# Kernel tuning notes

Hardware: AMD Instinct MI355X
Metric: run time of the kernel (lower is better)

## Reference

```python
import jax, jax.numpy as jnp
import numpy as np

# geomloss SamplesLoss(loss='sinkhorn', p=2, blur=0.05, scaling=0.8) constants
P = 2
BLUR = 0.05
SCALING = 0.8
# inputs are L2-normalized, so the point-cloud diameter is bounded by 2
DIAMETER = 2.0


def _eps_list():
    # geomloss epsilon_schedule: anneal eps from diameter**p down to blur**p
    e = [DIAMETER ** P]
    e += [float(np.exp(v)) for v in np.arange(P * np.log(DIAMETER), P * np.log(BLUR), P * np.log(SCALING))]
    e += [BLUR ** P]
    return e


def _cost(a, b):
    # geomloss p=2 cost: 0.5 * squared Euclidean distance, shape [N, M]
    sq = jnp.sum(a * a, -1)[:, None] + jnp.sum(b * b, -1)[None, :] - 2.0 * (a @ b.T)
    return 0.5 * jnp.maximum(sq, 0.0)


def _softmin(eps, C, h):
    # h = log-weights + potential/eps over the reduced axis; returns [N]
    return -eps * jax.nn.logsumexp(h[None, :] - C / eps, axis=1)


def _sinkhorn_divergence(x, y):
    # Debiased Sinkhorn divergence with epsilon-scaling (geomloss sinkhorn_tensorized)
    sg = jax.lax.stop_gradient
    N, M = x.shape[0], y.shape[0]
    a_log = jnp.full((N,), -np.log(N), x.dtype)  # uniform weights 1/N (log)
    b_log = jnp.full((M,), -np.log(M), y.dtype)

    C_xy = _cost(x, y)
    C_yx = C_xy.T
    C_xx = _cost(x, x)
    C_yy = _cost(y, y)
    # Sinkhorn loop runs without gradient (envelope theorem), like torch no_grad
    D_xy, D_yx, D_xx, D_yy = sg(C_xy), sg(C_yx), sg(C_xx), sg(C_yy)

    eps_list = _eps_list()
    eps = eps_list[0]
    g_ab = _softmin(eps, D_yx, a_log)   # potential on y for OT(a, b)
    f_ba = _softmin(eps, D_xy, b_log)   # potential on x for OT(a, b)
    f_aa = _softmin(eps, D_xx, a_log)   # debiasing potential OT(a, a)
    g_bb = _softmin(eps, D_yy, b_log)   # debiasing potential OT(b, b)

    for eps in eps_list:
        ft_ba = _softmin(eps, D_xy, b_log + g_ab / eps)
        gt_ab = _softmin(eps, D_yx, a_log + f_ba / eps)
        ft_aa = _softmin(eps, D_xx, a_log + f_aa / eps)
        gt_bb = _softmin(eps, D_yy, b_log + g_bb / eps)
        f_ba = 0.5 * (f_ba + ft_ba)
        g_ab = 0.5 * (g_ab + gt_ab)
        f_aa = 0.5 * (f_aa + ft_aa)
        g_bb = 0.5 * (g_bb + gt_bb)

    # final extrapolation with gradients enabled, dual potentials detached
    eps = eps_list[-1]
    f_ba, g_ab = (
        _softmin(eps, C_xy, sg(b_log + g_ab / eps)),
        _softmin(eps, C_yx, sg(a_log + f_ba / eps)),
    )
    f_aa = _softmin(eps, C_xx, sg(a_log + f_aa / eps))
    g_bb = _softmin(eps, C_yy, sg(b_log + g_bb / eps))

    # S_eps(a,b) = <a, f_ba - f_aa> + <b, g_ab - g_bb>, uniform weights
    return jnp.mean(f_ba - f_aa) + jnp.mean(g_ab - g_bb)


def setup_inputs() -> dict:
    key = jax.random.key(0)
    kx, ky = jax.random.split(key)
    x = jax.random.normal(kx, (4096, 64), jnp.float32)
    y = jax.random.normal(ky, (4096, 64), jnp.float32)
    return {"x": x, "y": y}


def reference(x, y):
    x = x / jnp.linalg.norm(x, axis=1, keepdims=True)
    y = y / jnp.linalg.norm(y, axis=1, keepdims=True)
    return _sinkhorn_divergence(x, y)
```

## Files before the change

kernel.cpp:

```cpp
#include <hip/hip_runtime.h>
#include <math.h>

#define NPTS 4096
#define DIM 64
#define NM ((size_t)NPTS * (size_t)NPTS)
#define LOGW (-8.317766166719343f)
#define NEGINF (-__builtin_inff())

typedef __bf16 bf16x8 __attribute__((ext_vector_type(8)));
typedef float f32x4 __attribute__((ext_vector_type(4)));
typedef _Float16 half8 __attribute__((ext_vector_type(8)));

static __device__ __forceinline__ f32x4 mfma16(bf16x8 a, bf16x8 b, f32x4 c) {
  return __builtin_amdgcn_mfma_f32_16x16x32_bf16(a, b, c, 0, 0, 0);
}

__global__ __launch_bounds__(256) void norm_split_kernel(
    const float* __restrict__ x, const float* __restrict__ y,
    __bf16* __restrict__ xh, __bf16* __restrict__ xl,
    __bf16* __restrict__ yh, __bf16* __restrict__ yl) {
  int row  = blockIdx.x * 4 + (threadIdx.x >> 6);
  int lane = threadIdx.x & 63;
  const float* src; __bf16 *dh, *dl;
  if (row < NPTS) {
    src = x + (size_t)row * DIM; dh = xh + (size_t)row * DIM; dl = xl + (size_t)row * DIM;
  } else {
    int r = row - NPTS;
    src = y + (size_t)r * DIM; dh = yh + (size_t)r * DIM; dl = yl + (size_t)r * DIM;
  }
  float v = src[lane];
  float s = v * v;
  #pragma unroll
  for (int o = 32; o; o >>= 1) s += __shfl_xor(s, o, 64);
  v *= 1.0f / sqrtf(s);
  __bf16 h = (__bf16)v;
  __bf16 l = (__bf16)(v - (float)h);
  dh[lane] = h;
  dl[lane] = l;
}

__global__ __launch_bounds__(256) void cost_mfma_kernel(
    const __bf16* __restrict__ xh, const __bf16* __restrict__ xl,
    const __bf16* __restrict__ yh, const __bf16* __restrict__ yl,
    _Float16* __restrict__ Cw) {
  int mat = blockIdx.z;
  const __bf16 *Ah, *Al, *Bh, *Bl;
  if (mat == 0)      { Ah = xh; Al = xl; Bh = yh; Bl = yl; }
  else if (mat == 1) { Ah = yh; Al = yl; Bh = xh; Bl = xl; }
  else if (mat == 2) { Ah = xh; Al = xl; Bh = xh; Bl = xl; }
  else               { Ah = yh; Al = yl; Bh = yh; Bl = yl; }
  _Float16* Cout = Cw + (size_t)mat * NM;

  int i0 = blockIdx.y * 64, j0 = blockIdx.x * 64;
  int wave = threadIdx.x >> 6, L = threadIdx.x & 63;
  int mrow = L & 15, quad = L >> 4;

  size_t abase = (size_t)(i0 + wave * 16 + mrow) * DIM + quad * 8;
  bf16x8 ah0 = *(const bf16x8*)(Ah + abase);
  bf16x8 ah1 = *(const bf16x8*)(Ah + abase + 32);
  bf16x8 al0 = *(const bf16x8*)(Al + abase);
  bf16x8 al1 = *(const bf16x8*)(Al + abase + 32);

  #pragma unroll
  for (int ct = 0; ct < 4; ++ct) {
    size_t bbase = (size_t)(j0 + ct * 16 + mrow) * DIM + quad * 8;
    bf16x8 bh0 = *(const bf16x8*)(Bh + bbase);
    bf16x8 bh1 = *(const bf16x8*)(Bh + bbase + 32);
    bf16x8 bl0 = *(const bf16x8*)(Bl + bbase);
    bf16x8 bl1 = *(const bf16x8*)(Bl + bbase + 32);
    f32x4 acc = {0.0f, 0.0f, 0.0f, 0.0f};
    acc = mfma16(ah0, bh0, acc);
    acc = mfma16(ah1, bh1, acc);
    acc = mfma16(al0, bh0, acc);
    acc = mfma16(al1, bh1, acc);
    acc = mfma16(ah0, bl0, acc);
    acc = mfma16(ah1, bl1, acc);
    int gj = j0 + ct * 16 + mrow;
    #pragma unroll
    for (int q = 0; q < 4; ++q) {
      int gi = i0 + wave * 16 + quad * 4 + q;
      Cout[(size_t)gi * NPTS + gj] = (_Float16)fmaxf(1.0f - acc[q], 0.0f);
    }
  }
}

__global__ __launch_bounds__(256) void pass_kernel(
    const _Float16* __restrict__ Cw,
    const float* __restrict__ potOld, float* __restrict__ potNew,
    float inv_eps, float eps, int use_pot, int avg) {
  int blk  = blockIdx.x;
  int mat  = blk >> 10;
  int row  = (blk & 1023) * 4 + (threadIdx.x >> 6);
  int lane = threadIdx.x & 63;
  const _Float16* Crow = Cw + (size_t)mat * NM + (size_t)row * NPTS;
  int ridx = (mat == 0) ? 1 : ((mat == 1) ? 0 : mat);
  const float* pot = potOld + (size_t)ridx * NPTS;

  float m0 = NEGINF, s0 = 0.0f, m1 = NEGINF, s1 = 0.0f;
  #pragma unroll 2
  for (int t = 0; t < 8; ++t) {
    int j = lane * 8 + t * 512;
    half8 c8 = *(const half8*)(Crow + j);
    float h[8];
    if (use_pot) {
      float4 pa = *(const float4*)(pot + j);
      float4 pb = *(const float4*)(pot + j + 4);
      h[0] = fmaf(pa.x, inv_eps, LOGW); h[1] = fmaf(pa.y, inv_eps, LOGW);
      h[2] = fmaf(pa.z, inv_eps, LOGW); h[3] = fmaf(pa.w, inv_eps, LOGW);
      h[4] = fmaf(pb.x, inv_eps, LOGW); h[5] = fmaf(pb.y, inv_eps, LOGW);
      h[6] = fmaf(pb.z, inv_eps, LOGW); h[7] = fmaf(pb.w, inv_eps, LOGW);
    } else {
      #pragma unroll
      for (int e = 0; e < 8; ++e) h[e] = LOGW;
    }
    #pragma unroll
    for (int e = 0; e < 8; e += 2) {
      float tv = fmaf((float)c8[e], -inv_eps, h[e]);
      float mn = fmaxf(m0, tv);
      s0 = s0 * __expf(m0 - mn) + __expf(tv - mn);
      m0 = mn;
      float tv1 = fmaf((float)c8[e + 1], -inv_eps, h[e + 1]);
      float mn1 = fmaxf(m1, tv1);
      s1 = s1 * __expf(m1 - mn1) + __expf(tv1 - mn1);
      m1 = mn1;
    }
  }
  {
    float mn = fmaxf(m0, m1);
    s0 = s0 * __expf(m0 - mn) + s1 * __expf(m1 - mn);
    m0 = mn;
  }
  #pragma unroll
  for (int o = 1; o < 64; o <<= 1) {
    float m2 = __shfl_xor(m0, o, 64);
    float s2 = __shfl_xor(s0, o, 64);
    float mn = fmaxf(m0, m2);
    s0 = s0 * __expf(m0 - mn) + s2 * __expf(m2 - mn);
    m0 = mn;
  }
  if (lane == 0) {
    float ft = -eps * (m0 + __logf(s0));
    float v = avg ? 0.5f * (potOld[(size_t)mat * NPTS + row] + ft) : ft;
    potNew[(size_t)mat * NPTS + row] = v;
  }
}

__global__ __launch_bounds__(256) void final_kernel(
    const float* __restrict__ pot, float* __restrict__ out) {
  __shared__ float red[256];
  float s = 0.0f;
  for (int j = threadIdx.x; j < NPTS; j += 256)
    s += (pot[j] - pot[2 * NPTS + j]) + (pot[NPTS + j] - pot[3 * NPTS + j]);
  red[threadIdx.x] = s;
  __syncthreads();
  #pragma unroll
  for (int o = 128; o; o >>= 1) {
    if (threadIdx.x < o) red[threadIdx.x] += red[threadIdx.x + o];
    __syncthreads();
  }
  if (threadIdx.x == 0) out[0] = red[0] / (float)NPTS;
}

extern "C" void kernel_launch(void* const* d_in, const int* in_sizes, int n_in,
                              void* d_out, int out_size, void* d_ws, size_t ws_size,
                              hipStream_t stream) {
  const float* x = (const float*)d_in[0];
  const float* y = (const float*)d_in[1];
  char* ws = (char*)d_ws;

  _Float16* Cw = (_Float16*)ws;
  __bf16* xh = (__bf16*)(ws + 4 * NM * sizeof(_Float16));
  __bf16* xl = xh + (size_t)NPTS * DIM;
  __bf16* yh = xl + (size_t)NPTS * DIM;
  __bf16* yl = yh + (size_t)NPTS * DIM;
  float* potA = (float*)(yl + (size_t)NPTS * DIM);
  float* potB = potA + 4 * (size_t)NPTS;
  size_t needed = (size_t)((char*)(potB + 4 * (size_t)NPTS) - ws);
  if (ws_size < needed) return;

  norm_split_kernel<<<2048, 256, 0, stream>>>(x, y, xh, xl, yh, yl);
  cost_mfma_kernel<<<dim3(64, 64, 4), 256, 0, stream>>>(xh, xl, yh, yl, Cw);

  double lst[32];
  int c = 0;
  lst[c++] = 4.0;
  double start = 2.0 * log(2.0), stop = 2.0 * log(0.05), step = 2.0 * log(0.8);
  for (int k = 0;; ++k) {
    double v = start + (double)k * step;
    if (v <= stop) break;
    lst[c++] = exp(v);
  }
  lst[c++] = 0.05 * 0.05;

  for (int p = 0; p < c + 2; ++p) {
    double e = (p == 0) ? lst[0] : ((p <= c) ? lst[p - 1] : lst[c - 1]);
    float eps = (float)e;
    float inv_eps = 1.0f / eps;
    int use_pot = (p > 0) ? 1 : 0;
    int avg = (p >= 1 && p <= c) ? 1 : 0;
    const float* po = (p & 1) ? potB : potA;
    float* pn       = (p & 1) ? potA : potB;
    pass_kernel<<<4096, 256, 0, stream>>>(Cw, po, pn, inv_eps, eps, use_pot, avg);
  }
  final_kernel<<<1, 256, 0, stream>>>(potB, (float*)d_out);
}
```

Measured before the change: 819.3 us.

## Fuse cost-matrix computation into each Sinkhorn pass, dropping stored cost matrices

Removes the precomputed fp16 cost matrices and recomputes the split-bf16 MFMA dot products inside each softmin pass, feeding an online logsumexp with a lazy max-rescale threshold. Each block handles 64 rows with the A fragments held in registers, streams B rows with one-step prefetch, and merges results across waves through LDS. This trades roughly 128 MB of HBM traffic per pass for extra matrix-core work, and runs with only one block per CU.

```diff
diff --git a/kernel.cpp b/kernel.cpp
--- a/kernel.cpp
+++ b/kernel.cpp
@@ -3,13 +3,11 @@
 
 #define NPTS 4096
 #define DIM 64
-#define NM ((size_t)NPTS * (size_t)NPTS)
 #define LOGW (-8.317766166719343f)
 #define NEGINF (-__builtin_inff())
 
 typedef __bf16 bf16x8 __attribute__((ext_vector_type(8)));
 typedef float f32x4 __attribute__((ext_vector_type(4)));
-typedef _Float16 half8 __attribute__((ext_vector_type(8)));
 
 static __device__ __forceinline__ f32x4 mfma16(bf16x8 a, bf16x8 b, f32x4 c) {
   return __builtin_amdgcn_mfma_f32_16x16x32_bf16(a, b, c, 0, 0, 0);
@@ -39,109 +37,135 @@
   dl[lane] = l;
 }
 
-__global__ __launch_bounds__(256) void cost_mfma_kernel(
+__global__ __launch_bounds__(256, 1) void fused_pass_kernel(
     const __bf16* __restrict__ xh, const __bf16* __restrict__ xl,
     const __bf16* __restrict__ yh, const __bf16* __restrict__ yl,
-    _Float16* __restrict__ Cw) {
-  int mat = blockIdx.z;
+    const float* __restrict__ potOld, float* __restrict__ potNew,
+    float inv_eps, float eps, int use_pot, int avg) {
+  __shared__ float hlds[NPTS];
+  __shared__ float mred[4][64];
+  __shared__ float sred[4][64];
+
+  int mat = blockIdx.x >> 6;
+  int rb  = blockIdx.x & 63;
   const __bf16 *Ah, *Al, *Bh, *Bl;
   if (mat == 0)      { Ah = xh; Al = xl; Bh = yh; Bl = yl; }
   else if (mat == 1) { Ah = yh; Al = yl; Bh = xh; Bl = xl; }
   else if (mat == 2) { Ah = xh; Al = xl; Bh = xh; Bl = xl; }
   else               { Ah = yh; Al = yl; Bh = yh; Bl = yl; }
-  _Float16* Cout = Cw + (size_t)mat * NM;
-
-  int i0 = blockIdx.y * 64, j0 = blockIdx.x * 64;
+  int ridx = (mat == 0) ? 1 : ((mat == 1) ? 0 : mat);
+  const float* pot = potOld + (size_t)ridx * NPTS;
+
+  for (int j4 = threadIdx.x; j4 < NPTS / 4; j4 += 256) {
+    float4 p;
+    if (use_pot) {
+      float4 q = *(const float4*)(pot + j4 * 4);
+      p.x = fmaf(q.x, inv_eps, LOGW); p.y = fmaf(q.y, inv_eps, LOGW);
+      p.z = fmaf(q.z, inv_eps, LOGW); p.w = fmaf(q.w, inv_eps, LOGW);
+    } else {
+      p.x = p.y = p.z = p.w = LOGW;
+    }
+    *(float4*)(hlds + j4 * 4) = p;
+  }
+  __syncthreads();
+
   int wave = threadIdx.x >> 6, L = threadIdx.x & 63;
   int mrow = L & 15, quad = L >> 4;
-
-  size_t abase = (size_t)(i0 + wave * 16 + mrow) * DIM + quad * 8;
-  bf16x8 ah0 = *(const bf16x8*)(Ah + abase);
-  bf16x8 ah1 = *(const bf16x8*)(Ah + abase + 32);
-  bf16x8 al0 = *(const bf16x8*)(Al + abase);
-  bf16x8 al1 = *(const bf16x8*)(Al + abase + 32);
-
-  #pragma unroll
-  for (int ct = 0; ct < 4; ++ct) {
-    size_t bbase = (size_t)(j0 + ct * 16 + mrow) * DIM + quad * 8;
-    bf16x8 bh0 = *(const bf16x8*)(Bh + bbase);
-    bf16x8 bh1 = *(const bf16x8*)(Bh + bbase + 32);
-    bf16x8 bl0 = *(const bf16x8*)(Bl + bbase);
-    bf16x8 bl1 = *(const bf16x8*)(Bl + bbase + 32);
-    f32x4 acc = {0.0f, 0.0f, 0.0f, 0.0f};
-    acc = mfma16(ah0, bh0, acc);
-    acc = mfma16(ah1, bh1, acc);
-    acc = mfma16(al0, bh0, acc);
-    acc = mfma16(al1, bh1, acc);
-    acc = mfma16(ah0, bl0, acc);
-    acc = mfma16(ah1, bl1, acc);
-    int gj = j0 + ct * 16 + mrow;
-    #pragma unroll
-    for (int q = 0; q < 4; ++q) {
-      int gi = i0 + wave * 16 + quad * 4 + q;
-      Cout[(size_t)gi * NPTS + gj] = (_Float16)fmaxf(1.0f - acc[q], 0.0f);
-    }
-  }
-}
-
-__global__ __launch_bounds__(256) void pass_kernel(
-    const _Float16* __restrict__ Cw,
-    const float* __restrict__ potOld, float* __restrict__ potNew,
-    float inv_eps, float eps, int use_pot, int avg) {
-  int blk  = blockIdx.x;
-  int mat  = blk >> 10;
-  int row  = (blk & 1023) * 4 + (threadIdx.x >> 6);
-  int lane = threadIdx.x & 63;
-  const _Float16* Crow = Cw + (size_t)mat * NM + (size_t)row * NPTS;
-  int ridx = (mat == 0) ? 1 : ((mat == 1) ? 0 : mat);
-  const float* pot = potOld + (size_t)ridx * NPTS;
-
-  float m0 = NEGINF, s0 = 0.0f, m1 = NEGINF, s1 = 0.0f;
-  #pragma unroll 2
-  for (int t = 0; t < 8; ++t) {
-    int j = lane * 8 + t * 512;
-    half8 c8 = *(const half8*)(Crow + j);
-    float h[8];
-    if (use_pot) {
-      float4 pa = *(const float4*)(pot + j);
-      float4 pb = *(const float4*)(pot + j + 4);
-      h[0] = fmaf(pa.x, inv_eps, LOGW); h[1] = fmaf(pa.y, inv_eps, LOGW);
-      h[2] = fmaf(pa.z, inv_eps, LOGW); h[3] = fmaf(pa.w, inv_eps, LOGW);
-      h[4] = fmaf(pb.x, inv_eps, LOGW); h[5] = fmaf(pb.y, inv_eps, LOGW);
-      h[6] = fmaf(pb.z, inv_eps, LOGW); h[7] = fmaf(pb.w, inv_eps, LOGW);
-    } else {
+  int i0 = rb * 64;
+
+  bf16x8 Afh0[4], Afh1[4], Afl0[4], Afl1[4];
+  #pragma unroll
+  for (int r = 0; r < 4; ++r) {
+    size_t ab = (size_t)(i0 + r * 16 + mrow) * DIM + quad * 8;
+    Afh0[r] = *(const bf16x8*)(Ah + ab);
+    Afh1[r] = *(const bf16x8*)(Ah + ab + 32);
+    Afl0[r] = *(const bf16x8*)(Al + ab);
+    Afl1[r] = *(const bf16x8*)(Al + ab + 32);
+  }
+
+  float sm[16], ss[16];
+  #pragma unroll
+  for (int i = 0; i < 16; ++i) { sm[i] = NEGINF; ss[i] = 0.0f; }
+
+  int jw = wave * 1024;
+  size_t bb = (size_t)(jw + mrow) * DIM + quad * 8;
+  bf16x8 b_h0 = *(const bf16x8*)(Bh + bb);
+  bf16x8 b_h1 = *(const bf16x8*)(Bh + bb + 32);
+  bf16x8 b_l0 = *(const bf16x8*)(Bl + bb);
+  bf16x8 b_l1 = *(const bf16x8*)(Bl + bb + 32);
+  float hh = hlds[jw + mrow];
+
+  for (int t = 0; t < 64; ++t) {
+    int tn = (t < 63) ? t + 1 : 63;
+    size_t bbn = (size_t)(jw + tn * 16 + mrow) * DIM + quad * 8;
+    bf16x8 n_h0 = *(const bf16x8*)(Bh + bbn);
+    bf16x8 n_h1 = *(const bf16x8*)(Bh + bbn + 32);
+    bf16x8 n_l0 = *(const bf16x8*)(Bl + bbn);
+    bf16x8 n_l1 = *(const bf16x8*)(Bl + bbn + 32);
+    float hhn = hlds[jw + tn * 16 + mrow];
+    float hp = hh - inv_eps;
+
+    #pragma unroll
+    for (int r = 0; r < 4; ++r) {
+      f32x4 acc = {0.0f, 0.0f, 0.0f, 0.0f};
+      acc = mfma16(Afh0[r], b_h0, acc);
+      acc = mfma16(Afh1[r], b_h1, acc);
+      acc = mfma16(Afl0[r], b_h0, acc);
+      acc = mfma16(Afl1[r], b_h1, acc);
+      acc = mfma16(Afh0[r], b_l0, acc);
+      acc = mfma16(Afh1[r], b_l1, acc);
       #pragma unroll
-      for (int e = 0; e < 8; ++e) h[e] = LOGW;
-    }
-    #pragma unroll
-    for (int e = 0; e < 8; e += 2) {
-      float tv = fmaf((float)c8[e], -inv_eps, h[e]);
-      float mn = fmaxf(m0, tv);
-      s0 = s0 * __expf(m0 - mn) + __expf(tv - mn);
-      m0 = mn;
-      float tv1 = fmaf((float)c8[e + 1], -inv_eps, h[e + 1]);
-      float mn1 = fmaxf(m1, tv1);
-      s1 = s1 * __expf(m1 - mn1) + __expf(tv1 - mn1);
-      m1 = mn1;
-    }
-  }
-  {
-    float mn = fmaxf(m0, m1);
-    s0 = s0 * __expf(m0 - mn) + s1 * __expf(m1 - mn);
-    m0 = mn;
-  }
-  #pragma unroll
-  for (int o = 1; o < 64; o <<= 1) {
-    float m2 = __shfl_xor(m0, o, 64);
-    float s2 = __shfl_xor(s0, o, 64);
-    float mn = fmaxf(m0, m2);
-    s0 = s0 * __expf(m0 - mn) + s2 * __expf(m2 - mn);
-    m0 = mn;
-  }
-  if (lane == 0) {
-    float ft = -eps * (m0 + __logf(s0));
-    float v = avg ? 0.5f * (potOld[(size_t)mat * NPTS + row] + ft) : ft;
-    potNew[(size_t)mat * NPTS + row] = v;
+      for (int q = 0; q < 4; ++q) {
+        float tv = fmaf(fminf(acc[q], 1.0f), inv_eps, hp);
+        int id = r * 4 + q;
+        float d = tv - sm[id];
+        bool big = d > 8.0f;
+        float e = __expf(big ? -d : d);
+        ss[id] = big ? fmaf(ss[id], e, 1.0f) : (ss[id] + e);
+        sm[id] = big ? tv : sm[id];
+      }
+    }
+    b_h0 = n_h0; b_h1 = n_h1; b_l0 = n_l0; b_l1 = n_l1;
+    hh = hhn;
+  }
+
+  #pragma unroll
+  for (int o = 1; o < 16; o <<= 1) {
+    #pragma unroll
+    for (int i = 0; i < 16; ++i) {
+      float m2 = __shfl_xor(sm[i], o, 64);
+      float s2 = __shfl_xor(ss[i], o, 64);
+      float mn = fmaxf(sm[i], m2);
+      ss[i] = ss[i] * __expf(sm[i] - mn) + s2 * __expf(m2 - mn);
+      sm[i] = mn;
+    }
+  }
+
+  if (mrow == 0) {
+    #pragma unroll
+    for (int r = 0; r < 4; ++r)
+      #pragma unroll
+      for (int q = 0; q < 4; ++q) {
+        int row = r * 16 + quad * 4 + q;
+        mred[wave][row] = sm[r * 4 + q];
+        sred[wave][row] = ss[r * 4 + q];
+      }
+  }
+  __syncthreads();
+
+  if (threadIdx.x < 64) {
+    int row = threadIdx.x;
+    float m = mred[0][row], s = sred[0][row];
+    #pragma unroll
+    for (int w = 1; w < 4; ++w) {
+      float m2 = mred[w][row], s2 = sred[w][row];
+      float mn = fmaxf(m, m2);
+      s = s * __expf(m - mn) + s2 * __expf(m2 - mn);
+      m = mn;
+    }
+    float ft = -eps * (m + __logf(s));
+    float v = avg ? 0.5f * (potOld[(size_t)mat * NPTS + i0 + row] + ft) : ft;
+    potNew[(size_t)mat * NPTS + i0 + row] = v;
   }
 }
 
@@ -168,8 +192,7 @@
   const float* y = (const float*)d_in[1];
   char* ws = (char*)d_ws;
 
-  _Float16* Cw = (_Float16*)ws;
-  __bf16* xh = (__bf16*)(ws + 4 * NM * sizeof(_Float16));
+  __bf16* xh = (__bf16*)ws;
   __bf16* xl = xh + (size_t)NPTS * DIM;
   __bf16* yh = xl + (size_t)NPTS * DIM;
   __bf16* yl = yh + (size_t)NPTS * DIM;
@@ -179,7 +202,6 @@
   if (ws_size < needed) return;
 
   norm_split_kernel<<<2048, 256, 0, stream>>>(x, y, xh, xl, yh, yl);
-  cost_mfma_kernel<<<dim3(64, 64, 4), 256, 0, stream>>>(xh, xl, yh, yl, Cw);
 
   double lst[32];
   int c = 0;
@@ -200,7 +222,8 @@
     int avg = (p >= 1 && p <= c) ? 1 : 0;
     const float* po = (p & 1) ? potB : potA;
     float* pn       = (p & 1) ? potA : potB;
-    pass_kernel<<<4096, 256, 0, stream>>>(Cw, po, pn, inv_eps, eps, use_pot, avg);
+    fused_pass_kernel<<<256, 256, 0, stream>>>(xh, xl, yh, yl, po, pn,
+                                               inv_eps, eps, use_pot, avg);
   }
   final_kernel<<<1, 256, 0, stream>>>(potB, (float*)d_out);
 }
```

Result: slower. 968.2 us (+18.2%).
